# Performance work log

Hardware: AMD Instinct MI355X
Metric: run time of the kernel (lower is better)

## Reference

```python
import jax, jax.numpy as jnp
import numpy as np
from jax import lax

T, B, S, D, V = 128, 512, 128, 128, 50257


def setup_inputs() -> dict:
    key = jax.random.key(0)
    ks = jax.random.split(key, 6)
    words = jax.random.randint(ks[0], (T, B), 0, V, dtype=jnp.int64)
    masks = jnp.ones((T, B), dtype=jnp.float32)
    tparams = jax.random.normal(ks[1], (S, S), dtype=jnp.float32)
    tag_embed = jax.random.normal(ks[2], (S, D), dtype=jnp.float32)
    word_embed = jax.random.normal(ks[3], (V, D), dtype=jnp.float32)
    transform = jax.random.normal(ks[4], (D, D), dtype=jnp.float32) * 0.05 + jnp.eye(D, dtype=jnp.float32)
    correction = jax.random.normal(ks[5], (S, V), dtype=jnp.float32) * 0.05
    return {"words": words, "masks": masks, "tparams": tparams,
            "tag_embed": tag_embed, "word_embed": word_embed,
            "transform": transform, "correction": correction}


def reference(words, masks, tparams, tag_embed, word_embed, transform, correction):
    num_state = tparams.shape[0]
    # update_emission (unsupervised mode): project word embeddings, score against tags,
    # add correction, log_softmax over the vocab dimension (dim=0 of (V,S)).
    word_emb = word_embed @ transform                      # (V, D)
    log_emission = jax.nn.log_softmax(word_emb @ tag_embed.T + correction.T, axis=0)  # (V, S)
    # _calc_logA: log-normalized transition matrix (rows = source state)
    logA = jax.nn.log_softmax(tparams, axis=1)             # (S, S)
    # uniform log prior pi = log(1/S)
    log_pi = jnp.full((num_state,), jnp.log(1.0 / num_state), dtype=log_emission.dtype)

    em = log_emission[words]                               # (T, B, S) gathered densities

    alpha0 = log_pi[None, :] + em[0]                       # (B, S)

    def step(alpha, inp):
        dens, m = inp                                      # (B,S), (B,)
        # _forward_cell: logsumexp over previous state of alpha + logA + density
        new = jax.nn.logsumexp(alpha[:, :, None] + logA[None, :, :] + dens[:, None, :], axis=1)
        m = m[:, None]
        alpha = m * new + (1.0 - m) * alpha
        return alpha, None

    alpha, _ = lax.scan(step, alpha0, (em[1:], masks[1:]))
    objective = jnp.sum(jax.nn.logsumexp(alpha, axis=1))
    return -objective
```

## Files before the change

### kernel.cpp

```cpp
#include <hip/hip_runtime.h>
#include <math.h>

#define T_ 128
#define B_ 512
#define S_ 128
#define D_ 128
#define V_ 50257

#define K2_VT 64
#define K2_NB ((V_ + K2_VT - 1) / K2_VT)

__global__ __launch_bounds__(128) void k1_m2(const float* __restrict__ transform,
                                             const float* __restrict__ tag_embed,
                                             float* __restrict__ M2) {
  __shared__ float te[128][129];
  int tid = threadIdx.x;
  for (int r = 0; r < 128; ++r) te[r][tid] = tag_embed[r * 128 + tid];
  __syncthreads();
  int k = blockIdx.x;
  float acc = 0.f;
  #pragma unroll 8
  for (int d = 0; d < 128; ++d) acc += transform[k * 128 + d] * te[tid][d];
  M2[k * 128 + tid] = acc;
}

__global__ __launch_bounds__(64) void k1b_a(const float* __restrict__ tparams,
                                            float* __restrict__ A) {
  int i = blockIdx.x;
  int l = threadIdx.x;
  float x0 = tparams[i * 128 + l];
  float x1 = tparams[i * 128 + 64 + l];
  float m = fmaxf(x0, x1);
  #pragma unroll
  for (int off = 32; off; off >>= 1) m = fmaxf(m, __shfl_xor(m, off));
  float e0 = __expf(x0 - m), e1 = __expf(x1 - m);
  float s = e0 + e1;
  #pragma unroll
  for (int off = 32; off; off >>= 1) s += __shfl_xor(s, off);
  float inv = 1.f / s;
  A[i * 128 + l]      = e0 * inv;
  A[i * 128 + 64 + l] = e1 * inv;
}

__global__ __launch_bounds__(256) void k2_logits(const float* __restrict__ we,
                                                 const float* __restrict__ M2,
                                                 const float* __restrict__ corr,
                                                 float* __restrict__ logits,
                                                 float* __restrict__ pmaxb,
                                                 float* __restrict__ psumb) {
  int tid = threadIdx.x;
  int sc = tid & 31;
  int vg = tid >> 5;
  long v0 = (long)blockIdx.x * K2_VT;
  __shared__ float weT[128][68];
  __shared__ float m2t[64][128];

  #pragma unroll
  for (int it = 0; it < 32; ++it) {
    int idx = it * 256 + tid;
    int d = idx & 127;
    int vv = idx >> 7;
    long v = v0 + vv;
    weT[d][vv] = (v < V_) ? we[v * 128 + d] : 0.f;
  }

  float acc[8][4];
  #pragma unroll
  for (int u = 0; u < 8; ++u)
    #pragma unroll
    for (int e = 0; e < 4; ++e) acc[u][e] = 0.f;

  #pragma unroll
  for (int c = 0; c < 2; ++c) {
    __syncthreads();
    #pragma unroll
    for (int it = 0; it < 32; ++it) {
      int idx = it * 256 + tid;
      int kr = idx >> 7, s = idx & 127;
      m2t[kr][s] = M2[(c * 64 + kr) * 128 + s];
    }
    __syncthreads();
    #pragma unroll 8
    for (int k = 0; k < 64; ++k) {
      float4 mv = *(const float4*)&m2t[k][4 * sc];
      float4 w0 = *(const float4*)&weT[c * 64 + k][8 * vg];
      float4 w1 = *(const float4*)&weT[c * 64 + k][8 * vg + 4];
      acc[0][0] += w0.x * mv.x; acc[0][1] += w0.x * mv.y; acc[0][2] += w0.x * mv.z; acc[0][3] += w0.x * mv.w;
      acc[1][0] += w0.y * mv.x; acc[1][1] += w0.y * mv.y; acc[1][2] += w0.y * mv.z; acc[1][3] += w0.y * mv.w;
      acc[2][0] += w0.z * mv.x; acc[2][1] += w0.z * mv.y; acc[2][2] += w0.z * mv.z; acc[2][3] += w0.z * mv.w;
      acc[3][0] += w0.w * mv.x; acc[3][1] += w0.w * mv.y; acc[3][2] += w0.w * mv.z; acc[3][3] += w0.w * mv.w;
      acc[4][0] += w1.x * mv.x; acc[4][1] += w1.x * mv.y; acc[4][2] += w1.x * mv.z; acc[4][3] += w1.x * mv.w;
      acc[5][0] += w1.y * mv.x; acc[5][1] += w1.y * mv.y; acc[5][2] += w1.y * mv.z; acc[5][3] += w1.y * mv.w;
      acc[6][0] += w1.z * mv.x; acc[6][1] += w1.z * mv.y; acc[6][2] += w1.z * mv.z; acc[6][3] += w1.z * mv.w;
      acc[7][0] += w1.w * mv.x; acc[7][1] += w1.w * mv.y; acc[7][2] += w1.w * mv.z; acc[7][3] += w1.w * mv.w;
    }
  }

  float lm[4], ls[4], Lst[8][4];
  #pragma unroll
  for (int e = 0; e < 4; ++e) { lm[e] = -INFINITY; ls[e] = 0.f; }
  long vbase = v0 + 8 * vg;
  #pragma unroll
  for (int e = 0; e < 4; ++e) {
    long rbase = (long)(4 * sc + e) * V_ + vbase;
    #pragma unroll
    for (int u = 0; u < 8; ++u) {
      if (vbase + u < V_) {
        float L = acc[u][e] + corr[rbase + u];
        Lst[u][e] = L;
        float nm = fmaxf(lm[e], L);
        ls[e] = ls[e] * __expf(lm[e] - nm) + __expf(L - nm);
        lm[e] = nm;
      }
    }
  }
  #pragma unroll
  for (int u = 0; u < 8; ++u) {
    long v = vbase + u;
    if (v < V_) {
      float4 st = make_float4(Lst[u][0], Lst[u][1], Lst[u][2], Lst[u][3]);
      *(float4*)&logits[v * 128 + 4 * sc] = st;
    }
  }

  __syncthreads();
  float* pmx = (float*)m2t;
  float* psm = pmx + 8 * 128;
  #pragma unroll
  for (int e = 0; e < 4; ++e) {
    pmx[vg * 128 + 4 * sc + e] = lm[e];
    psm[vg * 128 + 4 * sc + e] = ls[e];
  }
  __syncthreads();
  if (tid < 128) {
    int s = tid;
    float m = -INFINITY, sum = 0.f;
    #pragma unroll
    for (int g = 0; g < 8; ++g) {
      float pm = pmx[g * 128 + s];
      if (pm > -1e30f) {
        float ps = psm[g * 128 + s];
        float nm = fmaxf(m, pm);
        sum = sum * __expf(m - nm) + ps * __expf(pm - nm);
        m = nm;
      }
    }
    pmaxb[blockIdx.x * 128 + s] = m;
    psumb[blockIdx.x * 128 + s] = sum;
  }
}

__global__ __launch_bounds__(256) void k3_c(const float* __restrict__ pmaxb,
                                            const float* __restrict__ psumb,
                                            float* __restrict__ C) {
  int s = blockIdx.x;
  int t = threadIdx.x;
  float m = -INFINITY, sum = 0.f;
  #pragma unroll
  for (int q = 0; q < 4; ++q) {
    int b = t + q * 256;
    if (b < K2_NB) {
      float pm = pmaxb[b * 128 + s];
      if (pm > -1e30f) {
        float ps = psumb[b * 128 + s];
        float nm = fmaxf(m, pm);
        sum = sum * __expf(m - nm) + ps * __expf(pm - nm);
        m = nm;
      }
    }
  }
  #pragma unroll
  for (int off = 32; off; off >>= 1) {
    float om = __shfl_xor(m, off);
    float os = __shfl_xor(sum, off);
    float nm = fmaxf(m, om);
    sum = sum * __expf(m - nm) + os * __expf(om - nm);
    m = nm;
  }
  __shared__ float wm[4], wsv[4];
  int lane = t & 63, wv = t >> 6;
  if (lane == 0) { wm[wv] = m; wsv[wv] = sum; }
  __syncthreads();
  if (t == 0) {
    float M = fmaxf(fmaxf(wm[0], wm[1]), fmaxf(wm[2], wm[3]));
    float S = wsv[0] * __expf(wm[0] - M) + wsv[1] * __expf(wm[1] - M)
            + wsv[2] * __expf(wm[2] - M) + wsv[3] * __expf(wm[3] - M);
    C[s] = M + __logf(S);
  }
}

__global__ __launch_bounds__(512) void k4_rec(const int* __restrict__ words,
                                              const float* __restrict__ masks,
                                              const float* __restrict__ A,
                                              const float* __restrict__ C,
                                              const float* __restrict__ logits,
                                              float* __restrict__ bv) {
  const float kB = 70.70101247f;
  int tid = threadIdx.x;
  int j = tid & 127;
  int h = tid >> 7;
  int b = blockIdx.x;
  int lane = tid & 63, w = tid >> 6;
  __shared__ __align__(16) float els[128];
  __shared__ float part[4][128];
  __shared__ __align__(16) float pmax4[4];
  __shared__ float wred[2];
  __shared__ int   wbuf[128];
  __shared__ float mbuf[128];
  if (tid < 128) {
    wbuf[j] = words[j * B_ + b];
    mbuf[j] = masks[j * B_ + b];
  }
  float Ac[32];
  #pragma unroll
  for (int k = 0; k < 32; ++k) Ac[k] = A[(h * 32 + k) * 128 + j];
  __syncthreads();

  float a = 0.f, S = 0.f, em_cur = 0.f, Lnext = 0.f, Cj = 0.f, a0 = 0.f;
  if (tid < 128) {
    Cj = C[j];
    a0 = -4.852030263919617f + logits[(long)wbuf[0] * 128 + j] - Cj;
    float wm = a0;
    #pragma unroll
    for (int off = 32; off; off >>= 1) wm = fmaxf(wm, __shfl_xor(wm, off));
    if (lane == 0) wred[w] = wm;
  }
  __syncthreads();
  if (tid < 128) {
    float M0 = fmaxf(wred[0], wred[1]);
    a = __expf(a0 - M0);
    S = M0;
    els[j] = a;
    float L1 = logits[(long)wbuf[1] * 128 + j];
    Lnext    = logits[(long)wbuf[2] * 128 + j];
    em_cur = __expf(L1 - Cj + kB);
  }
  __syncthreads();

  for (int t = 1; t < T_; ++t) {
    float4 e0 = ((const float4*)els)[h * 8 + 0];
    float4 e1 = ((const float4*)els)[h * 8 + 1];
    float4 e2 = ((const float4*)els)[h * 8 + 2];
    float4 e3 = ((const float4*)els)[h * 8 + 3];
    float4 e4 = ((const float4*)els)[h * 8 + 4];
    float4 e5 = ((const float4*)els)[h * 8 + 5];
    float4 e6 = ((const float4*)els)[h * 8 + 6];
    float4 e7 = ((const float4*)els)[h * 8 + 7];
    float p0 = e0.x * Ac[0]  + e0.y * Ac[1]  + e0.z * Ac[2]  + e0.w * Ac[3]
             + e1.x * Ac[4]  + e1.y * Ac[5]  + e1.z * Ac[6]  + e1.w * Ac[7];
    float p1 = e2.x * Ac[8]  + e2.y * Ac[9]  + e2.z * Ac[10] + e2.w * Ac[11]
             + e3.x * Ac[12] + e3.y * Ac[13] + e3.z * Ac[14] + e3.w * Ac[15];
    float p2 = e4.x * Ac[16] + e4.y * Ac[17] + e4.z * Ac[18] + e4.w * Ac[19]
             + e5.x * Ac[20] + e5.y * Ac[21] + e5.z * Ac[22] + e5.w * Ac[23];
    float p3 = e6.x * Ac[24] + e6.y * Ac[25] + e6.z * Ac[26] + e6.w * Ac[27]
             + e7.x * Ac[28] + e7.y * Ac[29] + e7.z * Ac[30] + e7.w * Ac[31];
    part[h][j] = (p0 + p1) + (p2 + p3);
    if (j == 0) {
      float4 ma = make_float4(fmaxf(e0.x, e1.x), fmaxf(e0.y, e1.y), fmaxf(e0.z, e1.z), fmaxf(e0.w, e1.w));
      float4 mb = make_float4(fmaxf(e2.x, e3.x), fmaxf(e2.y, e3.y), fmaxf(e2.z, e3.z), fmaxf(e2.w, e3.w));
      float4 mc = make_float4(fmaxf(e4.x, e5.x), fmaxf(e4.y, e5.y), fmaxf(e4.z, e5.z), fmaxf(e4.w, e5.w));
      float4 md = make_float4(fmaxf(e6.x, e7.x), fmaxf(e6.y, e7.y), fmaxf(e6.z, e7.z), fmaxf(e6.w, e7.w));
      float4 m1 = make_float4(fmaxf(ma.x, mb.x), fmaxf(ma.y, mb.y), fmaxf(ma.z, mb.z), fmaxf(ma.w, mb.w));
      float4 m2 = make_float4(fmaxf(mc.x, md.x), fmaxf(mc.y, md.y), fmaxf(mc.z, md.z), fmaxf(mc.w, md.w));
      float mx = fmaxf(fmaxf(fmaxf(m1.x, m1.y), fmaxf(m1.z, m1.w)),
                       fmaxf(fmaxf(m2.x, m2.y), fmaxf(m2.z, m2.w)));
      pmax4[h] = mx;
    }
    float em_next = 0.f, Lf = 0.f;
    if (tid < 128) {
      if (t + 2 < T_) Lf = logits[(long)wbuf[t + 2] * 128 + j];
      em_next = __expf(Lnext - Cj + kB);
    }
    __syncthreads();
    if (tid < 128) {
      float4 pm4 = *(const float4*)pmax4;
      float Mst = fmaxf(fmaxf(pm4.x, pm4.y), fmaxf(pm4.z, pm4.w));
      float invM = 1.f / Mst;
      float P = (part[0][j] + part[1][j]) + (part[2][j] + part[3][j]);
      float nv   = (P * invM) * em_cur;
      float oldq = (a * invM) * 0x1p102f;
      float mm = mbuf[t];
      a = mm * nv + (1.f - mm) * oldq;
      els[j] = a;
      S += __logf(Mst) - kB;
      em_cur = em_next;
      Lnext = Lf;
    }
    __syncthreads();
  }

  if (tid < 128) {
    float ss = a;
    #pragma unroll
    for (int off = 32; off; off >>= 1) ss += __shfl_xor(ss, off);
    if (lane == 0) wred[w] = ss;
  }
  __syncthreads();
  if (tid == 0) bv[b] = S + __logf(wred[0] + wred[1]);
}

__global__ __launch_bounds__(256) void k5_sum(const float* __restrict__ bv,
                                              float* __restrict__ out) {
  int t = threadIdx.x;
  float s = bv[t] + bv[t + 256];
  #pragma unroll
  for (int off = 32; off; off >>= 1) s += __shfl_xor(s, off);
  __shared__ float wsm[4];
  if ((t & 63) == 0) wsm[t >> 6] = s;
  __syncthreads();
  if (t == 0) out[0] = -(wsm[0] + wsm[1] + wsm[2] + wsm[3]);
}

extern "C" void kernel_launch(void* const* d_in, const int* in_sizes, int n_in,
                              void* d_out, int out_size, void* d_ws, size_t ws_size,
                              hipStream_t stream) {
  const int*   words      = (const int*)d_in[0];
  const float* masks      = (const float*)d_in[1];
  const float* tparams    = (const float*)d_in[2];
  const float* tag_embed  = (const float*)d_in[3];
  const float* word_embed = (const float*)d_in[4];
  const float* transform  = (const float*)d_in[5];
  const float* correction = (const float*)d_in[6];

  float* ws     = (float*)d_ws;
  float* M2     = ws;
  float* A      = ws + 16384;
  float* C      = ws + 32768;
  float* bv     = ws + 32896;
  float* pmaxb  = ws + 33408;
  float* psumb  = ws + 134016;
  float* logits = ws + 234624;

  hipLaunchKernelGGL(k1_m2,    dim3(128),    dim3(128), 0, stream, transform, tag_embed, M2);
  hipLaunchKernelGGL(k1b_a,    dim3(128),    dim3(64),  0, stream, tparams, A);
  hipLaunchKernelGGL(k2_logits,dim3(K2_NB),  dim3(256), 0, stream, word_embed, M2, correction, logits, pmaxb, psumb);
  hipLaunchKernelGGL(k3_c,     dim3(S_),     dim3(256), 0, stream, pmaxb, psumb, C);
  hipLaunchKernelGGL(k4_rec,   dim3(512),    dim3(512), 0, stream, words, masks, A, C, logits, bv);
  hipLaunchKernelGGL(k5_sum,   dim3(1),      dim3(256), 0, stream, bv, (float*)d_out);
}
```

Measured before the change: 193.7 us.

## Prefetch all emission gathers into LDS before recurrence, add occupancy hints

Before the time loop starts, the recurrence kernel now gathers and exponentiates every per-step emission value into a 64KB shared-memory table, using all 512 threads. This takes the dependent global loads out of the serial 127-step loop, which now only reads from LDS. Launch bounds with minimum-block hints are added to the logits and recurrence kernels. The large LDS allocation limits how many blocks fit per CU, and the occupancy hints may force register spilling.

Result: no change. 194.8 us (+0.5%).

```diff
diff --git a/kernel.cpp b/kernel.cpp
--- a/kernel.cpp
+++ b/kernel.cpp
@@ -42,7 +42,7 @@
   A[i * 128 + 64 + l] = e1 * inv;
 }
 
-__global__ __launch_bounds__(256) void k2_logits(const float* __restrict__ we,
+__global__ __launch_bounds__(256, 2) void k2_logits(const float* __restrict__ we,
                                                  const float* __restrict__ M2,
                                                  const float* __restrict__ corr,
                                                  float* __restrict__ logits,
@@ -189,7 +189,7 @@
   }
 }
 
-__global__ __launch_bounds__(512) void k4_rec(const int* __restrict__ words,
+__global__ __launch_bounds__(512, 4) void k4_rec(const int* __restrict__ words,
                                               const float* __restrict__ masks,
                                               const float* __restrict__ A,
                                               const float* __restrict__ C,
@@ -207,6 +207,7 @@
   __shared__ float wred[2];
   __shared__ int   wbuf[128];
   __shared__ float mbuf[128];
+  __shared__ float em[127 * 128];
   if (tid < 128) {
     wbuf[j] = words[j * B_ + b];
     mbuf[j] = masks[j * B_ + b];
@@ -214,12 +215,21 @@
   float Ac[32];
   #pragma unroll
   for (int k = 0; k < 32; ++k) Ac[k] = A[(h * 32 + k) * 128 + j];
-  __syncthreads();
-
-  float a = 0.f, S = 0.f, em_cur = 0.f, Lnext = 0.f, Cj = 0.f, a0 = 0.f;
-  if (tid < 128) {
-    Cj = C[j];
-    a0 = -4.852030263919617f + logits[(long)wbuf[0] * 128 + j] - Cj;
+  float Cj = C[j];
+  __syncthreads();
+
+  #pragma unroll 4
+  for (int tt = 0; tt < 32; ++tt) {
+    int t = tt * 4 + h;
+    if (t >= 1) {
+      float L = logits[(unsigned)(wbuf[t] * 128 + j)];
+      em[(t - 1) * 128 + j] = __expf(L - Cj + kB);
+    }
+  }
+
+  float a = 0.f, S = 0.f, a0 = 0.f;
+  if (tid < 128) {
+    a0 = -4.852030263919617f + logits[(unsigned)(wbuf[0] * 128 + j)] - Cj;
     float wm = a0;
     #pragma unroll
     for (int off = 32; off; off >>= 1) wm = fmaxf(wm, __shfl_xor(wm, off));
@@ -231,9 +241,6 @@
     a = __expf(a0 - M0);
     S = M0;
     els[j] = a;
-    float L1 = logits[(long)wbuf[1] * 128 + j];
-    Lnext    = logits[(long)wbuf[2] * 128 + j];
-    em_cur = __expf(L1 - Cj + kB);
   }
   __syncthreads();
 
@@ -266,10 +273,10 @@
                        fmaxf(fmaxf(m2.x, m2.y), fmaxf(m2.z, m2.w)));
       pmax4[h] = mx;
     }
-    float em_next = 0.f, Lf = 0.f;
+    float emv = 0.f, mm = 0.f;
     if (tid < 128) {
-      if (t + 2 < T_) Lf = logits[(long)wbuf[t + 2] * 128 + j];
-      em_next = __expf(Lnext - Cj + kB);
+      emv = em[(t - 1) * 128 + j];
+      mm = mbuf[t];
     }
     __syncthreads();
     if (tid < 128) {
@@ -277,14 +284,11 @@
       float Mst = fmaxf(fmaxf(pm4.x, pm4.y), fmaxf(pm4.z, pm4.w));
       float invM = 1.f / Mst;
       float P = (part[0][j] + part[1][j]) + (part[2][j] + part[3][j]);
-      float nv   = (P * invM) * em_cur;
+      float nv   = (P * invM) * emv;
       float oldq = (a * invM) * 0x1p102f;
-      float mm = mbuf[t];
       a = mm * nv + (1.f - mm) * oldq;
       els[j] = a;
       S += __logf(Mst) - kB;
-      em_cur = em_next;
-      Lnext = Lf;
     }
     __syncthreads();
   }
```
